# Performance work log

Measured on AMD Instinct MI355X. Metric: run time of the kernel, lower is better.

Reference implementation:

```python
import jax, jax.numpy as jnp
import numpy as np

EPS = 1e-6  # GLOBAL_EPS
D_QK = 192
ATTN_DIM = 768


def setup_inputs() -> dict:
    key = jax.random.key(0)
    ks = jax.random.split(key, 12)
    B, C, H, W = 16, 192, 56, 56
    d_qk, d_v = D_QK, 2 * D_QK
    attn_dim, inner = ATTN_DIM, d_v
    r = lambda k, s, sc=0.05: jax.random.normal(k, s, dtype=jnp.float32) * sc
    return {
        "x": jax.random.normal(ks[0], (B, C, H, W), dtype=jnp.float32),
        "proj_w": r(ks[1], (attn_dim, C)),          # 1x1 conv + BN folded
        "proj_b": r(ks[2], (attn_dim,)),
        "dwc_w": r(ks[3], (attn_dim, 1, 3, 3)),     # depthwise 3x3, BN folded
        "dwc_b": r(ks[4], (attn_dim,)),
        "g_w": r(ks[5], (inner, attn_dim)),          # ConvGate pointwise conv1d
        "g_b": r(ks[6], (inner,)),
        "an_w": 1.0 + r(ks[7], (inner,)),            # RMSNorm weight
        "sv": 1.0 + r(ks[8], (inner,)),              # Scale(inner, (1, inner, 1))
        "out_w": r(ks[9], (C, inner)),               # 1x1 conv + BN folded
        "out_b": r(ks[10], (C,)),
    }


def reference(x, proj_w, proj_b, dwc_w, dwc_b, g_w, g_b, an_w, sv, out_w, out_b):
    B, C, H, W = x.shape
    d_qk = D_QK
    # proj: ConvNorm 1x1 (conv + BN folded to affine)
    y = jnp.einsum("bchw,oc->bohw", x, proj_w) + proj_b[None, :, None, None]
    # dwc: RepConv depthwise 3x3 with residual (res=True)
    dw = jax.lax.conv_general_dilated(
        y, dwc_w, window_strides=(1, 1), padding="SAME",
        dimension_numbers=("NCHW", "OIHW", "NCHW"),
        feature_group_count=ATTN_DIM)
    y = dw + dwc_b[None, :, None, None] + y
    # flatten spatial -> tokens, split q/k/v along channels
    xs = y.reshape(B, ATTN_DIM, H * W)            # (B, attn_dim, N)
    q, k, v = xs[:, :d_qk], xs[:, d_qk:2 * d_qk], xs[:, 2 * d_qk:]
    # linear_attn: feature map = silu, scale = N**-0.5
    qf = jax.nn.silu(q)                            # (B, d_qk, N)
    kf = jax.nn.silu(k)
    N = H * W
    s = N ** -0.5
    # use_linear branch (N >> d): z = kT.mean(-2,True) @ q + eps ; attn = (v s)(kT s) q
    z = jnp.einsum("bd,bdn->bn", kf.mean(-1), qf)[:, None, :] + EPS  # (B, 1, N)
    vk = jnp.einsum("bvn,bdn->bvd", v * s, kf * s)  # (B, d_v, d_qk)
    attn = jnp.einsum("bvd,bdn->bvn", vk, qf) / z   # (B, d_v, N)
    # gate: pointwise conv1d on full projected features + sigmoid
    gate = jax.nn.sigmoid(jnp.einsum("bcn,oc->bon", xs, g_w) + g_b[None, :, None])
    attn = attn * gate
    # attn_norm (RMS over channels) + scale_v(v) residual
    rms = jnp.sqrt(jnp.mean(attn * attn, axis=1, keepdims=True) + EPS)
    attn = attn / rms * an_w[None, :, None] + v * sv[None, :, None]
    # out: ConvNorm 1x1 back to dim
    o = attn.reshape(B, -1, H, W)
    return jnp.einsum("bchw,oc->bohw", o, out_w) + out_b[None, :, None, None]
```

## Files before the change

kernel.cpp:

```cpp
#include <hip/hip_runtime.h>
#include <hip/hip_bf16.h>

typedef unsigned short u16;
typedef __attribute__((ext_vector_type(8))) short bf16x8;
typedef __attribute__((ext_vector_type(4))) float f32x4;

constexpr int B_ = 16, C_ = 192, H_ = 56, W_ = 56;
constexpr int N_ = H_ * W_;
constexpr int A_ = 768;
constexpr int Dq = 192;
constexpr int Vd = 384;
constexpr float EPSf = 1e-6f;

union U8 { bf16x8 v; u16 s[8]; unsigned u[4]; };

__device__ __forceinline__ float bits2f(u16 u) {
  return __uint_as_float(((unsigned)u) << 16);
}
__device__ __forceinline__ u16 f2bits(float f) {
  __hip_bfloat16 h = __float2bfloat16(f);
  u16 u;
  __builtin_memcpy(&u, &h, sizeof(u));
  return u;
}
__device__ __forceinline__ float silu_f(float v) { return v / (1.0f + __expf(-v)); }
__device__ __forceinline__ float sigm_f(float v) { return 1.0f / (1.0f + __expf(-v)); }

__device__ __forceinline__ f32x4 MFMA(bf16x8 a, bf16x8 b, f32x4 c) {
  return __builtin_amdgcn_mfma_f32_16x16x32_bf16(a, b, c, 0, 0, 0);
}
__device__ __forceinline__ int swz(int row) { return (row & 7) ^ ((row >> 3) & 7); }

__global__ __launch_bounds__(256) void k_prep(const float* __restrict__ pw,
                                              const float* __restrict__ gw,
                                              const float* __restrict__ ow,
                                              u16* __restrict__ pwb,
                                              u16* __restrict__ gwb,
                                              u16* __restrict__ owb) {
  const int bid = blockIdx.x;
  const size_t base = ((size_t)bid * 256 + threadIdx.x) * 8;
  const float* src;
  u16* dst;
  size_t off;
  if (bid < 72) { src = pw; dst = pwb; off = base; }
  else if (bid < 216) { src = gw; dst = gwb; off = base - 147456; }
  else { src = ow; dst = owb; off = base - 442368; }
  float4 v0 = *(const float4*)&src[off];
  float4 v1 = *(const float4*)&src[off + 4];
  U8 r;
  r.s[0] = f2bits(v0.x); r.s[1] = f2bits(v0.y); r.s[2] = f2bits(v0.z); r.s[3] = f2bits(v0.w);
  r.s[4] = f2bits(v1.x); r.s[5] = f2bits(v1.y); r.s[6] = f2bits(v1.z); r.s[7] = f2bits(v1.w);
  *(bf16x8*)&dst[off] = r.v;
}

__global__ __launch_bounds__(256) void k_proj(const float* __restrict__ x,
                                              const u16* __restrict__ pwb,
                                              const float* __restrict__ pb,
                                              u16* __restrict__ y0t) {
  const int n0 = blockIdx.x * 64;
  const int oy = blockIdx.y;
  const int b = blockIdx.z;
  __shared__ u16 Xt[64][200];
  __shared__ u16 Wa[256][32];
  const int t = threadIdx.x;
  const int lane = t & 63, wid = t >> 6;
  const int fr = lane & 15, fg = lane >> 4;

  {
    const int p = t & 31, co = t >> 5;
    const float* xb = x + (size_t)b * C_ * N_ + n0 + 2 * p;
#pragma unroll
    for (int rnd = 0; rnd < 3; ++rnd) {
      const int c0 = rnd * 64 + co * 8;
      float2 v[8];
#pragma unroll
      for (int i = 0; i < 8; ++i) v[i] = *(const float2*)&xb[(size_t)(c0 + i) * N_];
      U8 r0, r1;
#pragma unroll
      for (int i = 0; i < 8; ++i) { r0.s[i] = f2bits(v[i].x); r1.s[i] = f2bits(v[i].y); }
      *(bf16x8*)&Xt[2 * p][c0] = r0.v;
      *(bf16x8*)&Xt[2 * p + 1][c0] = r1.v;
    }
  }

  f32x4 acc[4][4];
#pragma unroll
  for (int mi = 0; mi < 4; ++mi)
#pragma unroll
    for (int ni = 0; ni < 4; ++ni) acc[mi][ni] = (f32x4){0.f, 0.f, 0.f, 0.f};

  const int orow_c = t >> 2, oct_c = t & 3;
  U8 wreg[4];
#pragma unroll
  for (int jj = 0; jj < 4; ++jj)
    wreg[jj].v = *(const bf16x8*)&pwb[(size_t)(oy * 256 + orow_c + 64 * jj) * C_ + oct_c * 8];

  for (int ks = 0; ks < 6; ++ks) {
    __syncthreads();
#pragma unroll
    for (int jj = 0; jj < 4; ++jj) {
      const int orow = orow_c + 64 * jj;
      const int sw = (orow >> 1) & 3;
      *(bf16x8*)&Wa[orow][(oct_c ^ sw) * 8] = wreg[jj].v;
    }
    __syncthreads();
    if (ks < 5) {
#pragma unroll
      for (int jj = 0; jj < 4; ++jj)
        wreg[jj].v = *(const bf16x8*)&pwb[(size_t)(oy * 256 + orow_c + 64 * jj) * C_ +
                                          (ks + 1) * 32 + oct_c * 8];
    }
    bf16x8 bfrag[4];
#pragma unroll
    for (int ni = 0; ni < 4; ++ni)
      bfrag[ni] = *(const bf16x8*)&Xt[ni * 16 + fr][ks * 32 + fg * 8];
    __builtin_amdgcn_s_setprio(1);
#pragma unroll
    for (int mi = 0; mi < 4; ++mi) {
      const int ar = wid * 64 + mi * 16 + fr;
      bf16x8 a = *(const bf16x8*)&Wa[ar][(fg ^ ((ar >> 1) & 3)) * 8];
#pragma unroll
      for (int ni = 0; ni < 4; ++ni) acc[mi][ni] = MFMA(a, bfrag[ni], acc[mi][ni]);
    }
    __builtin_amdgcn_s_setprio(0);
  }
#pragma unroll
  for (int mi = 0; mi < 4; ++mi) {
    const int o4 = oy * 256 + wid * 64 + mi * 16 + fg * 4;
    const float b0 = pb[o4], b1 = pb[o4 + 1], b2 = pb[o4 + 2], b3 = pb[o4 + 3];
#pragma unroll
    for (int ni = 0; ni < 4; ++ni) {
      const int n = n0 + ni * 16 + fr;
      ushort4 pk;
      pk.x = f2bits(acc[mi][ni][0] + b0);
      pk.y = f2bits(acc[mi][ni][1] + b1);
      pk.z = f2bits(acc[mi][ni][2] + b2);
      pk.w = f2bits(acc[mi][ni][3] + b3);
      *(ushort4*)&y0t[((size_t)b * N_ + n) * A_ + o4] = pk;
    }
  }
}

__global__ __launch_bounds__(256) void k_dwc(const u16* __restrict__ y0t,
                                             const float* __restrict__ cw,
                                             const float* __restrict__ cb,
                                             u16* __restrict__ yt) {
  const int pid = blockIdx.x;
  const int L = (pid & 7) * 336 + (pid >> 3);
  const int h = L % 56, at = (L / 56) % 3, b = L / 168;
  const int t = threadIdx.x;
  const int a = at * 256 + (t & 31) * 8;
  const int wl = t >> 5;
  float w9[9][8];
  float bias[8];
#pragma unroll
  for (int j = 0; j < 8; ++j) {
    bias[j] = cb[a + j];
#pragma unroll
    for (int k = 0; k < 9; ++k) w9[k][j] = cw[(a + j) * 9 + k];
  }
  const u16* src = y0t + (size_t)b * N_ * A_ + a;
  u16* dst = yt + (size_t)b * N_ * A_ + a;
  const bool hok0 = h > 0, hok2 = h < 55;
  for (int wc = 0; wc < 7; ++wc) {
    const int w = wc * 8 + wl;
    const bool wok0 = w > 0, wok2 = w < 55;
    U8 nb[9];
#pragma unroll
    for (int dh = -1; dh <= 1; ++dh) {
      const bool hok = (dh == -1) ? hok0 : ((dh == 1) ? hok2 : true);
#pragma unroll
      for (int dw = -1; dw <= 1; ++dw) {
        const int k = (dh + 1) * 3 + (dw + 1);
        const bool ok = hok && ((dw == -1) ? wok0 : ((dw == 1) ? wok2 : true));
        if (ok)
          nb[k].v = *(const bf16x8*)&src[(size_t)((h + dh) * 56 + (w + dw)) * A_];
        else
          nb[k].u[0] = nb[k].u[1] = nb[k].u[2] = nb[k].u[3] = 0u;
      }
    }
    U8 o;
#pragma unroll
    for (int j = 0; j < 8; ++j) {
      float s = bias[j] + bits2f(nb[4].s[j]);
#pragma unroll
      for (int k = 0; k < 9; ++k) s = fmaf(w9[k][j], bits2f(nb[k].s[j]), s);
      o.s[j] = f2bits(s);
    }
    *(bf16x8*)&dst[(size_t)(h * 56 + w) * A_] = o.v;
  }
}

__global__ __launch_bounds__(256) void k_kfmean(const u16* __restrict__ yt,
                                                float* __restrict__ kfp) {
  const int ns = blockIdx.x, dc = blockIdx.y, b = blockIdx.z;
  const int t = threadIdx.x;
  const int dq = t & 15, nw = t >> 4;
  const u16* p = yt + ((size_t)b * N_ + ns * 448 + nw) * A_ + 192 + dc * 64 + dq * 4;
  float s0 = 0, s1 = 0, s2 = 0, s3 = 0;
#pragma unroll 4
  for (int i = 0; i < 28; ++i) {
    ushort4 u = *(const ushort4*)&p[(size_t)i * 16 * A_];
    s0 += silu_f(bits2f(u.x));
    s1 += silu_f(bits2f(u.y));
    s2 += silu_f(bits2f(u.z));
    s3 += silu_f(bits2f(u.w));
  }
  __shared__ float red[16][65];
  red[nw][dq * 4 + 0] = s0;
  red[nw][dq * 4 + 1] = s1;
  red[nw][dq * 4 + 2] = s2;
  red[nw][dq * 4 + 3] = s3;
  __syncthreads();
  if (t < 64) {
    float s = 0;
#pragma unroll
    for (int i = 0; i < 16; ++i) s += red[i][t];
    kfp[((size_t)ns * B_ + b) * Dq + dc * 64 + t] = s * (1.0f / (float)N_);
  }
}

__global__ __launch_bounds__(256) void k_z(const u16* __restrict__ yt,
                                           const float* __restrict__ kfp,
                                           float* __restrict__ zinv) {
  const int b = blockIdx.y;
  const int n = blockIdx.x * 256 + threadIdx.x;
  __shared__ float kf[192];
  if (threadIdx.x < 192) {
    float s = 0;
#pragma unroll
    for (int ns = 0; ns < 7; ++ns) s += kfp[((size_t)ns * B_ + b) * Dq + threadIdx.x];
    kf[threadIdx.x] = s;
  }
  __syncthreads();
  if (n < N_) {
    const u16* p = yt + ((size_t)b * N_ + n) * A_;
    float z = 0;
#pragma unroll
    for (int j = 0; j < 24; ++j) {
      U8 u;
      u.v = *(const bf16x8*)&p[j * 8];
#pragma unroll
      for (int i = 0; i < 8; ++i) z = fmaf(kf[j * 8 + i], silu_f(bits2f(u.s[i])), z);
    }
    zinv[(size_t)b * N_ + n] = 1.0f / (z + EPSf);
  }
}

__global__ __launch_bounds__(256) void k_vk(const u16* __restrict__ yt,
                                            float* __restrict__ vkpart) {
  const int pid = blockIdx.x;
  const int L = (pid & 7) * 42 + (pid >> 3);
  const int ns = L % 7;
  const int vblk = (L / 7) % 3;
  const int b = L / 21;
  const int t = threadIdx.x;
  const int lane = t & 63, wid = t >> 6;
  const int fr = lane & 15, fg = lane >> 4;
  const int vbase = (wid >> 1) * 64, dbase = (wid & 1) * 96;

  __shared__ u16 T[320 * 64];
  unsigned* T32 = (unsigned*)T;

  const int oct0 = t & 7;
  const int pair = (t >> 3) & 31;
  const int nb0 = ns * 448;

  U8 pre[5][2];
  auto load_pre = [&](int n0) {
    const int n = nb0 + n0 + pair * 2;
#pragma unroll
    for (int j = 0; j < 5; ++j) {
      const int oct = oct0 + 8 * j;
      const u16* srcp;
      if (j < 3)
        srcp = yt + ((size_t)b * N_ + n) * A_ + 192 + oct * 8;
      else
        srcp = yt + ((size_t)b * N_ + n) * A_ + 384 + vblk * 128 + (oct - 24) * 8;
      pre[j][0].v = *(const bf16x8*)srcp;
      pre[j][1].v = *(const bf16x8*)(srcp + A_);
      if (j < 3) {
#pragma unroll
        for (int i = 0; i < 8; ++i) {
          pre[j][0].s[i] = f2bits(silu_f(bits2f(pre[j][0].s[i])));
          pre[j][1].s[i] = f2bits(silu_f(bits2f(pre[j][1].s[i])));
        }
      }
    }
  };

  f32x4 acc[4][6];
#pragma unroll
  for (int mi = 0; mi < 4; ++mi)
#pragma unroll
    for (int ni = 0; ni < 6; ++ni) acc[mi][ni] = (f32x4){0.f, 0.f, 0.f, 0.f};

  load_pre(0);
  for (int s = 0; s < 7; ++s) {
    __syncthreads();
#pragma unroll
    for (int j = 0; j < 5; ++j) {
      const int rowb = (oct0 + 8 * j) * 8;
#pragma unroll
      for (int i = 0; i < 8; ++i) {
        const int row = rowb + i;
        const int sw = swz(row);
        const unsigned val =
            ((unsigned)pre[j][0].s[i] & 0xffffu) | (((unsigned)pre[j][1].s[i]) << 16);
        T32[row * 32 + (pair ^ (sw << 2))] = val;
      }
    }
    __syncthreads();
    if (s < 6) load_pre((s + 1) * 64);
    __builtin_amdgcn_s_setprio(1);
#pragma unroll
    for (int kf2 = 0; kf2 < 2; ++kf2) {
      bf16x8 bfrag[6];
#pragma unroll
      for (int ni = 0; ni < 6; ++ni) {
        const int row = dbase + ni * 16 + fr;
        bfrag[ni] = *(const bf16x8*)&T[row * 64 + ((kf2 * 32 + fg * 8) ^ (swz(row) << 3))];
      }
#pragma unroll
      for (int mi = 0; mi < 4; ++mi) {
        const int row = 192 + vbase + mi * 16 + fr;
        bf16x8 a = *(const bf16x8*)&T[row * 64 + ((kf2 * 32 + fg * 8) ^ (swz(row) << 3))];
#pragma unroll
        for (int ni = 0; ni < 6; ++ni) acc[mi][ni] = MFMA(a, bfrag[ni], acc[mi][ni]);
      }
    }
    __builtin_amdgcn_s_setprio(0);
  }
  float* base = vkpart + (((size_t)ns * 16 + b) * 3 + vblk) * (128 * 192);
#pragma unroll
  for (int mi = 0; mi < 4; ++mi)
#pragma unroll
    for (int ni = 0; ni < 6; ++ni) {
      const int v = vbase + mi * 16 + fg * 4;
      const int d = dbase + ni * 16 + fr;
      float* o = base + (size_t)v * 192 + d;
      o[0] = acc[mi][ni][0];
      o[192] = acc[mi][ni][1];
      o[384] = acc[mi][ni][2];
      o[576] = acc[mi][ni][3];
    }
}

__global__ __launch_bounds__(256) void k_vkred(const float* __restrict__ vkpart,
                                               u16* __restrict__ vkb) {
  const size_t e = ((size_t)blockIdx.x * 256 + threadIdx.x) * 8;
  constexpr size_t NSSTRIDE = (size_t)16 * 3 * 128 * 192;
  float4 s0 = {0, 0, 0, 0}, s1 = {0, 0, 0, 0};
#pragma unroll
  for (int ns = 0; ns < 7; ++ns) {
    float4 a0 = *(const float4*)&vkpart[ns * NSSTRIDE + e];
    float4 a1 = *(const float4*)&vkpart[ns * NSSTRIDE + e + 4];
    s0.x += a0.x; s0.y += a0.y; s0.z += a0.z; s0.w += a0.w;
    s1.x += a1.x; s1.y += a1.y; s1.z += a1.z; s1.w += a1.w;
  }
  const float sc = 1.0f / (float)N_;
  U8 r;
  r.s[0] = f2bits(s0.x * sc); r.s[1] = f2bits(s0.y * sc);
  r.s[2] = f2bits(s0.z * sc); r.s[3] = f2bits(s0.w * sc);
  r.s[4] = f2bits(s1.x * sc); r.s[5] = f2bits(s1.y * sc);
  r.s[6] = f2bits(s1.z * sc); r.s[7] = f2bits(s1.w * sc);
  *(bf16x8*)&vkb[e] = r.v;
}

__global__ __launch_bounds__(256) void k_gateattn(const u16* __restrict__ yt,
                                                  const float* __restrict__ zinv,
                                                  const u16* __restrict__ vkb,
                                                  const u16* __restrict__ gwb,
                                                  const float* __restrict__ gb,
                                                  u16* __restrict__ attnt) {
  const int pid = blockIdx.x;
  const int L = (pid & 7) * 196 + (pid >> 3);
  const int vh = L & 1;
  const int n0 = ((L >> 1) % 49) * 64;
  const int b = L / 98;
  const int t = threadIdx.x;
  const int lane = t & 63, wid = t >> 6, wm = wid >> 1, wn = wid & 1;
  const int fr = lane & 15, fg = lane >> 4;
  __shared__ u16 T[2][256 * 64];
  __shared__ float zl[64];
  if (t < 64) zl[t] = zinv[(size_t)b * N_ + n0 + t];
  const u16* yb = yt + ((size_t)b * N_ + n0) * A_;
  const u16* wb0 = vkb + ((size_t)b * Vd + vh * 192) * 192;
  const u16* wb1 = gwb + (size_t)(vh * 192) * A_;

  const int oct = t & 7, rowb = t >> 3;
  U8 pre[8];
  auto loadPre = [&](int nit) {
    if (nit < 3) {
      const int ks = nit * 64;
#pragma unroll
      for (int j = 0; j < 6; ++j)
        pre[j].v = *(const bf16x8*)&wb0[(size_t)(rowb + 32 * j) * 192 + ks + oct * 8];
#pragma unroll
      for (int j = 6; j < 8; ++j)
        pre[j].v = *(const bf16x8*)&yb[(size_t)(rowb + 32 * (j - 6)) * A_ + ks + oct * 8];
    } else {
      const int ks = (nit - 3) * 64;
#pragma unroll
      for (int j = 0; j < 6; ++j)
        pre[j].v = *(const bf16x8*)&wb1[(size_t)(rowb + 32 * j) * A_ + ks + oct * 8];
#pragma unroll
      for (int j = 6; j < 8; ++j)
        pre[j].v = *(const bf16x8*)&yb[(size_t)(rowb + 32 * (j - 6)) * A_ + ks + oct * 8];
    }
  };
  auto writeStage = [&](int nit, int buf) {
    const bool sl = (nit < 3);
    u16* Tb = &T[buf][0];
#pragma unroll
    for (int j = 0; j < 8; ++j) {
      const int r = rowb + 32 * j;
      U8 w = pre[j];
      if (sl && j >= 6) {
#pragma unroll
        for (int i = 0; i < 8; ++i) w.s[i] = f2bits(silu_f(bits2f(w.s[i])));
      }
      *(bf16x8*)&Tb[r * 64 + ((oct * 8) ^ (swz(r) << 3))] = w.v;
    }
  };

  f32x4 acc[6][2];
#pragma unroll
  for (int mi = 0; mi < 6; ++mi)
#pragma unroll
    for (int ni = 0; ni < 2; ++ni) acc[mi][ni] = (f32x4){0.f, 0.f, 0.f, 0.f};
  uint2 pp[6][2];

  loadPre(0);
  writeStage(0, 0);
  loadPre(1);
  __syncthreads();

  for (int it = 0; it < 15; ++it) {
    const int cur = it & 1;
    if (it < 14) writeStage(it + 1, cur ^ 1);
    if (it < 13) loadPre(it + 2);
    const u16* Tb = &T[cur][0];
    __builtin_amdgcn_s_setprio(1);
#pragma unroll
    for (int kf2 = 0; kf2 < 2; ++kf2) {
      bf16x8 bfr[2];
#pragma unroll
      for (int ni = 0; ni < 2; ++ni) {
        const int row = 192 + wn * 32 + ni * 16 + fr;
        bfr[ni] = *(const bf16x8*)&Tb[row * 64 + ((kf2 * 32 + fg * 8) ^ (swz(row) << 3))];
      }
#pragma unroll
      for (int mi = 0; mi < 6; ++mi) {
        const int row = wm * 96 + mi * 16 + fr;
        bf16x8 a = *(const bf16x8*)&Tb[row * 64 + ((kf2 * 32 + fg * 8) ^ (swz(row) << 3))];
        acc[mi][0] = MFMA(a, bfr[0], acc[mi][0]);
        acc[mi][1] = MFMA(a, bfr[1], acc[mi][1]);
      }
    }
    __builtin_amdgcn_s_setprio(0);
    if (it == 2) {
#pragma unroll
      for (int mi = 0; mi < 6; ++mi)
#pragma unroll
        for (int ni = 0; ni < 2; ++ni) {
          const float z = zl[wn * 32 + ni * 16 + fr];
          unsigned a0 = ((unsigned)f2bits(acc[mi][ni][0] * z) & 0xffffu) |
                        (((unsigned)f2bits(acc[mi][ni][1] * z) & 0xffffu) << 16);
          unsigned a1 = ((unsigned)f2bits(acc[mi][ni][2] * z) & 0xffffu) |
                        (((unsigned)f2bits(acc[mi][ni][3] * z) & 0xffffu) << 16);
          pp[mi][ni] = make_uint2(a0, a1);
          acc[mi][ni] = (f32x4){0.f, 0.f, 0.f, 0.f};
        }
    }
    __syncthreads();
  }

#pragma unroll
  for (int mi = 0; mi < 6; ++mi) {
    const int vb = vh * 192 + wm * 96 + mi * 16 + fg * 4;
    const float g0 = gb[vb], g1 = gb[vb + 1], g2 = gb[vb + 2], g3 = gb[vb + 3];
#pragma unroll
    for (int ni = 0; ni < 2; ++ni) {
      const int n = n0 + wn * 32 + ni * 16 + fr;
      const uint2 p = pp[mi][ni];
      const float pv0 = bits2f((u16)(p.x & 0xffffu)), pv1 = bits2f((u16)(p.x >> 16));
      const float pv2 = bits2f((u16)(p.y & 0xffffu)), pv3 = bits2f((u16)(p.y >> 16));
      ushort4 o;
      o.x = f2bits(pv0 * sigm_f(acc[mi][ni][0] + g0));
      o.y = f2bits(pv1 * sigm_f(acc[mi][ni][1] + g1));
      o.z = f2bits(pv2 * sigm_f(acc[mi][ni][2] + g2));
      o.w = f2bits(pv3 * sigm_f(acc[mi][ni][3] + g3));
      *(ushort4*)&attnt[((size_t)b * N_ + n) * Vd + vb] = o;
    }
  }
}

__global__ __launch_bounds__(256) void k_out(const u16* __restrict__ attnt,
                                             const u16* __restrict__ yt,
                                             const u16* __restrict__ owb,
                                             const float* __restrict__ ob,
                                             const float* __restrict__ anw,
                                             const float* __restrict__ svw,
                                             float* __restrict__ out) {
  const int n0 = blockIdx.x * 64;
  const int b = blockIdx.y;
  __shared__ u16 T[256 * 64];
  __shared__ float anws[384], svws[384];
  __shared__ float red[64][4];
  __shared__ float rinv[64];
  const int t = threadIdx.x;
  const int lane = t & 63, wid = t >> 6, wm = wid >> 1, wn = wid & 1;
  const int fr = lane & 15, fg = lane >> 4;
  for (int i = t; i < 384; i += 256) {
    anws[i] = anw[i];
    svws[i] = svw[i];
  }
  {
    const int n = t >> 2, q = t & 3;
    const u16* ab = attnt + ((size_t)b * N_ + n0 + n) * Vd;
    float ss = 0.f;
#pragma unroll
    for (int i = 0; i < 4; ++i) {
      U8 u, u2, u3;
      u.v = *(const bf16x8*)&ab[(q + 4 * i) * 8 + 0];
      u2.v = *(const bf16x8*)&ab[(q + 4 * i) * 8 + 128];
      u3.v = *(const bf16x8*)&ab[(q + 4 * i) * 8 + 256];
#pragma unroll
      for (int k = 0; k < 8; ++k) {
        float f0 = bits2f(u.s[k]), f1 = bits2f(u2.s[k]), f2 = bits2f(u3.s[k]);
        ss = fmaf(f0, f0, ss);
        ss = fmaf(f1, f1, ss);
        ss = fmaf(f2, f2, ss);
      }
    }
    red[n][q] = ss;
  }
  __syncthreads();
  if (t < 64)
    rinv[t] = rsqrtf((red[t][0] + red[t][1] + red[t][2] + red[t][3]) * (1.0f / (float)Vd) + EPSf);

  const int oct = t & 7, rowb = t >> 3;
  U8 preW[6], preA[2], preV[2];
  auto loadPre = [&](int it) {
    const int ks = it * 64;
#pragma unroll
    for (int j = 0; j < 6; ++j)
      preW[j].v = *(const bf16x8*)&owb[(size_t)(rowb + 32 * j) * Vd + ks + oct * 8];
#pragma unroll
    for (int j = 0; j < 2; ++j) {
      const int n = rowb + 32 * j;
      preA[j].v = *(const bf16x8*)&attnt[((size_t)b * N_ + n0 + n) * Vd + ks + oct * 8];
      preV[j].v = *(const bf16x8*)&yt[((size_t)b * N_ + n0 + n) * A_ + 384 + ks + oct * 8];
    }
  };

  f32x4 acc[6][2];
#pragma unroll
  for (int mi = 0; mi < 6; ++mi)
#pragma unroll
    for (int ni = 0; ni < 2; ++ni) acc[mi][ni] = (f32x4){0.f, 0.f, 0.f, 0.f};

  loadPre(0);
  __syncthreads();
  for (int it = 0; it < 6; ++it) {
#pragma unroll
    for (int j = 0; j < 6; ++j) {
      const int r = rowb + 32 * j;
      *(bf16x8*)&T[r * 64 + ((oct * 8) ^ (swz(r) << 3))] = preW[j].v;
    }
#pragma unroll
    for (int j = 0; j < 2; ++j) {
      const int n = rowb + 32 * j;
      const int r = 192 + n;
      const float ri = rinv[n];
      const int col0 = it * 64 + oct * 8;
      U8 o;
#pragma unroll
      for (int k = 0; k < 8; ++k)
        o.s[k] = f2bits(bits2f(preA[j].s[k]) * ri * anws[col0 + k] +
                        bits2f(preV[j].s[k]) * svws[col0 + k]);
      *(bf16x8*)&T[r * 64 + ((oct * 8) ^ (swz(r) << 3))] = o.v;
    }
    __syncthreads();
    if (it < 5) loadPre(it + 1);
    __builtin_amdgcn_s_setprio(1);
#pragma unroll
    for (int kf2 = 0; kf2 < 2; ++kf2) {
      bf16x8 bfr[2];
#pragma unroll
      for (int ni = 0; ni < 2; ++ni) {
        const int row = 192 + wn * 32 + ni * 16 + fr;
        bfr[ni] = *(const bf16x8*)&T[row * 64 + ((kf2 * 32 + fg * 8) ^ (swz(row) << 3))];
      }
#pragma unroll
      for (int mi = 0; mi < 6; ++mi) {
        const int row = wm * 96 + mi * 16 + fr;
        bf16x8 a = *(const bf16x8*)&T[row * 64 + ((kf2 * 32 + fg * 8) ^ (swz(row) << 3))];
        acc[mi][0] = MFMA(a, bfr[0], acc[mi][0]);
        acc[mi][1] = MFMA(a, bfr[1], acc[mi][1]);
      }
    }
    __builtin_amdgcn_s_setprio(0);
    if (it < 5) __syncthreads();
  }
#pragma unroll
  for (int mi = 0; mi < 6; ++mi) {
    const int c = wm * 96 + mi * 16 + fg * 4;
    const float b0 = ob[c], b1 = ob[c + 1], b2 = ob[c + 2], b3 = ob[c + 3];
#pragma unroll
    for (int ni = 0; ni < 2; ++ni) {
      const int n = n0 + wn * 32 + ni * 16 + fr;
      float* o = out + ((size_t)b * C_ + c) * N_ + n;
      o[0 * N_] = acc[mi][ni][0] + b0;
      o[1 * N_] = acc[mi][ni][1] + b1;
      o[2 * N_] = acc[mi][ni][2] + b2;
      o[3 * N_] = acc[mi][ni][3] + b3;
    }
  }
}

extern "C" void kernel_launch(void* const* d_in, const int* in_sizes, int n_in,
                              void* d_out, int out_size, void* d_ws, size_t ws_size,
                              hipStream_t stream) {
  (void)in_sizes; (void)n_in; (void)out_size; (void)ws_size;
  const float* x = (const float*)d_in[0];
  const float* pw = (const float*)d_in[1];
  const float* pb = (const float*)d_in[2];
  const float* cw = (const float*)d_in[3];
  const float* cb = (const float*)d_in[4];
  const float* gw = (const float*)d_in[5];
  const float* gb = (const float*)d_in[6];
  const float* anw = (const float*)d_in[7];
  const float* svw = (const float*)d_in[8];
  const float* ow = (const float*)d_in[9];
  const float* ob = (const float*)d_in[10];
  float* out = (float*)d_out;

  char* ws = (char*)d_ws;
  const size_t szY = (size_t)B_ * N_ * A_ * 2;
  u16* y0t = (u16*)(ws);
  u16* attnt = (u16*)(ws);
  float* vkpart = (float*)(ws + 38535168);
  u16* vkb = (u16*)(ws + 71565312);
  u16* yt = (u16*)(ws + szY);
  char* ws2 = ws + 2 * szY;
  float* kfp = (float*)(ws2);
  float* zinv = (float*)(ws2 + 86016);
  u16* pwb = (u16*)(ws2 + 86016 + 200704);
  u16* gwb = (u16*)(ws2 + 86016 + 200704 + 294912);
  u16* owb = (u16*)(ws2 + 86016 + 200704 + 294912 + 589824);

  k_prep<<<dim3(252), 256, 0, stream>>>(pw, gw, ow, pwb, gwb, owb);
  k_proj<<<dim3(49, 3, 16), 256, 0, stream>>>(x, pwb, pb, y0t);
  k_dwc<<<dim3(2688), 256, 0, stream>>>(y0t, cw, cb, yt);
  k_kfmean<<<dim3(7, 3, 16), 256, 0, stream>>>(yt, kfp);
  k_z<<<dim3(13, 16), 256, 0, stream>>>(yt, kfp, zinv);
  k_vk<<<dim3(336), 256, 0, stream>>>(yt, vkpart);
  k_vkred<<<dim3(576), 256, 0, stream>>>(vkpart, vkb);
  k_gateattn<<<dim3(1568), 256, 0, stream>>>(yt, zinv, vkb, gwb, gb, attnt);
  k_out<<<dim3(49, 16), 256, 0, stream>>>(attnt, yt, owb, ob, anw, svw, out);
}
```

Before: 264.3 us.

## Widen gate-attention token tile to 128 and fuse RMS sum-of-squares via atomics

The per-batch token stride is padded to 3200 so the gate/attention kernel can use 128-token tiles (800 blocks instead of 1568), doubling MFMA columns per wave and halving how often weight tiles are reloaded. The gate kernel now accumulates each token's sum of squares and adds it atomically into a buffer, which k_z zeroes beforehand. This removes the separate re-read of the attention output in k_out for the RMS norm. In exchange it needs more registers and LDS per block (launch bounds 2), computes on padded tokens (whose zinv is set to zero), and uses float atomics, so the summation order is no longer fixed.

```diff
diff --git a/kernel.cpp b/kernel.cpp
--- a/kernel.cpp
+++ b/kernel.cpp
@@ -7,6 +7,7 @@
 
 constexpr int B_ = 16, C_ = 192, H_ = 56, W_ = 56;
 constexpr int N_ = H_ * W_;
+constexpr int NP = 3200;
 constexpr int A_ = 768;
 constexpr int Dq = 192;
 constexpr int Vd = 384;
@@ -136,7 +137,7 @@
       pk.y = f2bits(acc[mi][ni][1] + b1);
       pk.z = f2bits(acc[mi][ni][2] + b2);
       pk.w = f2bits(acc[mi][ni][3] + b3);
-      *(ushort4*)&y0t[((size_t)b * N_ + n) * A_ + o4] = pk;
+      *(ushort4*)&y0t[((size_t)b * NP + n) * A_ + o4] = pk;
     }
   }
 }
@@ -159,8 +160,8 @@
 #pragma unroll
     for (int k = 0; k < 9; ++k) w9[k][j] = cw[(a + j) * 9 + k];
   }
-  const u16* src = y0t + (size_t)b * N_ * A_ + a;
-  u16* dst = yt + (size_t)b * N_ * A_ + a;
+  const u16* src = y0t + (size_t)b * NP * A_ + a;
+  u16* dst = yt + (size_t)b * NP * A_ + a;
   const bool hok0 = h > 0, hok2 = h < 55;
   for (int wc = 0; wc < 7; ++wc) {
     const int w = wc * 8 + wl;
@@ -196,7 +197,7 @@
   const int ns = blockIdx.x, dc = blockIdx.y, b = blockIdx.z;
   const int t = threadIdx.x;
   const int dq = t & 15, nw = t >> 4;
-  const u16* p = yt + ((size_t)b * N_ + ns * 448 + nw) * A_ + 192 + dc * 64 + dq * 4;
+  const u16* p = yt + ((size_t)b * NP + ns * 448 + nw) * A_ + 192 + dc * 64 + dq * 4;
   float s0 = 0, s1 = 0, s2 = 0, s3 = 0;
 #pragma unroll 4
   for (int i = 0; i < 28; ++i) {
@@ -222,7 +223,8 @@
 
 __global__ __launch_bounds__(256) void k_z(const u16* __restrict__ yt,
                                            const float* __restrict__ kfp,
-                                           float* __restrict__ zinv) {
+                                           float* __restrict__ zinv,
+                                           float* __restrict__ ssq) {
   const int b = blockIdx.y;
   const int n = blockIdx.x * 256 + threadIdx.x;
   __shared__ float kf[192];
@@ -233,17 +235,22 @@
     kf[threadIdx.x] = s;
   }
   __syncthreads();
-  if (n < N_) {
-    const u16* p = yt + ((size_t)b * N_ + n) * A_;
-    float z = 0;
-#pragma unroll
-    for (int j = 0; j < 24; ++j) {
-      U8 u;
-      u.v = *(const bf16x8*)&p[j * 8];
-#pragma unroll
-      for (int i = 0; i < 8; ++i) z = fmaf(kf[j * 8 + i], silu_f(bits2f(u.s[i])), z);
-    }
-    zinv[(size_t)b * N_ + n] = 1.0f / (z + EPSf);
+  if (n < NP) {
+    if (n < N_) {
+      const u16* p = yt + ((size_t)b * NP + n) * A_;
+      float z = 0;
+#pragma unroll
+      for (int j = 0; j < 24; ++j) {
+        U8 u;
+        u.v = *(const bf16x8*)&p[j * 8];
+#pragma unroll
+        for (int i = 0; i < 8; ++i) z = fmaf(kf[j * 8 + i], silu_f(bits2f(u.s[i])), z);
+      }
+      zinv[(size_t)b * NP + n] = 1.0f / (z + EPSf);
+    } else {
+      zinv[(size_t)b * NP + n] = 0.f;
+    }
+    ssq[(size_t)b * NP + n] = 0.f;
   }
 }
 
@@ -274,9 +281,9 @@
       const int oct = oct0 + 8 * j;
       const u16* srcp;
       if (j < 3)
-        srcp = yt + ((size_t)b * N_ + n) * A_ + 192 + oct * 8;
+        srcp = yt + ((size_t)b * NP + n) * A_ + 192 + oct * 8;
       else
-        srcp = yt + ((size_t)b * N_ + n) * A_ + 384 + vblk * 128 + (oct - 24) * 8;
+        srcp = yt + ((size_t)b * NP + n) * A_ + 384 + vblk * 128 + (oct - 24) * 8;
       pre[j][0].v = *(const bf16x8*)srcp;
       pre[j][1].v = *(const bf16x8*)(srcp + A_);
       if (j < 3) {
@@ -367,29 +374,28 @@
   *(bf16x8*)&vkb[e] = r.v;
 }
 
-__global__ __launch_bounds__(256) void k_gateattn(const u16* __restrict__ yt,
-                                                  const float* __restrict__ zinv,
-                                                  const u16* __restrict__ vkb,
-                                                  const u16* __restrict__ gwb,
-                                                  const float* __restrict__ gb,
-                                                  u16* __restrict__ attnt) {
+__global__ __launch_bounds__(256, 2) void k_gateattn(const u16* __restrict__ yt,
+                                                     const float* __restrict__ zinv,
+                                                     const u16* __restrict__ vkb,
+                                                     const u16* __restrict__ gwb,
+                                                     const float* __restrict__ gb,
+                                                     u16* __restrict__ attnt,
+                                                     float* __restrict__ ssq) {
   const int pid = blockIdx.x;
-  const int L = (pid & 7) * 196 + (pid >> 3);
+  const int L = (pid & 7) * 100 + (pid >> 3);
   const int vh = L & 1;
-  const int n0 = ((L >> 1) % 49) * 64;
-  const int b = L / 98;
+  const int n0 = ((L >> 1) % 25) * 128;
+  const int b = L / 50;
   const int t = threadIdx.x;
   const int lane = t & 63, wid = t >> 6, wm = wid >> 1, wn = wid & 1;
   const int fr = lane & 15, fg = lane >> 4;
-  __shared__ u16 T[2][256 * 64];
-  __shared__ float zl[64];
-  if (t < 64) zl[t] = zinv[(size_t)b * N_ + n0 + t];
-  const u16* yb = yt + ((size_t)b * N_ + n0) * A_;
+  __shared__ u16 T[2][320 * 64];
+  const u16* yb = yt + ((size_t)b * NP + n0) * A_;
   const u16* wb0 = vkb + ((size_t)b * Vd + vh * 192) * 192;
   const u16* wb1 = gwb + (size_t)(vh * 192) * A_;
 
   const int oct = t & 7, rowb = t >> 3;
-  U8 pre[8];
+  U8 pre[10];
   auto loadPre = [&](int nit) {
     if (nit < 3) {
       const int ks = nit * 64;
@@ -397,7 +403,7 @@
       for (int j = 0; j < 6; ++j)
         pre[j].v = *(const bf16x8*)&wb0[(size_t)(rowb + 32 * j) * 192 + ks + oct * 8];
 #pragma unroll
-      for (int j = 6; j < 8; ++j)
+      for (int j = 6; j < 10; ++j)
         pre[j].v = *(const bf16x8*)&yb[(size_t)(rowb + 32 * (j - 6)) * A_ + ks + oct * 8];
     } else {
       const int ks = (nit - 3) * 64;
@@ -405,7 +411,7 @@
       for (int j = 0; j < 6; ++j)
         pre[j].v = *(const bf16x8*)&wb1[(size_t)(rowb + 32 * j) * A_ + ks + oct * 8];
 #pragma unroll
-      for (int j = 6; j < 8; ++j)
+      for (int j = 6; j < 10; ++j)
         pre[j].v = *(const bf16x8*)&yb[(size_t)(rowb + 32 * (j - 6)) * A_ + ks + oct * 8];
     }
   };
@@ -413,7 +419,7 @@
     const bool sl = (nit < 3);
     u16* Tb = &T[buf][0];
 #pragma unroll
-    for (int j = 0; j < 8; ++j) {
+    for (int j = 0; j < 10; ++j) {
       const int r = rowb + 32 * j;
       U8 w = pre[j];
       if (sl && j >= 6) {
@@ -424,12 +430,12 @@
     }
   };
 
-  f32x4 acc[6][2];
+  f32x4 acc[6][4];
 #pragma unroll
   for (int mi = 0; mi < 6; ++mi)
 #pragma unroll
-    for (int ni = 0; ni < 2; ++ni) acc[mi][ni] = (f32x4){0.f, 0.f, 0.f, 0.f};
-  uint2 pp[6][2];
+    for (int ni = 0; ni < 4; ++ni) acc[mi][ni] = (f32x4){0.f, 0.f, 0.f, 0.f};
+  uint2 pp[6][4];
 
   loadPre(0);
   writeStage(0, 0);
@@ -444,27 +450,31 @@
     __builtin_amdgcn_s_setprio(1);
 #pragma unroll
     for (int kf2 = 0; kf2 < 2; ++kf2) {
-      bf16x8 bfr[2];
-#pragma unroll
-      for (int ni = 0; ni < 2; ++ni) {
-        const int row = 192 + wn * 32 + ni * 16 + fr;
+      bf16x8 bfr[4];
+#pragma unroll
+      for (int ni = 0; ni < 4; ++ni) {
+        const int row = 192 + wn * 64 + ni * 16 + fr;
         bfr[ni] = *(const bf16x8*)&Tb[row * 64 + ((kf2 * 32 + fg * 8) ^ (swz(row) << 3))];
       }
 #pragma unroll
       for (int mi = 0; mi < 6; ++mi) {
         const int row = wm * 96 + mi * 16 + fr;
         bf16x8 a = *(const bf16x8*)&Tb[row * 64 + ((kf2 * 32 + fg * 8) ^ (swz(row) << 3))];
-        acc[mi][0] = MFMA(a, bfr[0], acc[mi][0]);
-        acc[mi][1] = MFMA(a, bfr[1], acc[mi][1]);
+#pragma unroll
+        for (int ni = 0; ni < 4; ++ni) acc[mi][ni] = MFMA(a, bfr[ni], acc[mi][ni]);
       }
     }
     __builtin_amdgcn_s_setprio(0);
     if (it == 2) {
+      float zv[4];
+#pragma unroll
+      for (int ni = 0; ni < 4; ++ni)
+        zv[ni] = zinv[(size_t)b * NP + n0 + wn * 64 + ni * 16 + fr];
 #pragma unroll
       for (int mi = 0; mi < 6; ++mi)
 #pragma unroll
-        for (int ni = 0; ni < 2; ++ni) {
-          const float z = zl[wn * 32 + ni * 16 + fr];
+        for (int ni = 0; ni < 4; ++ni) {
+          const float z = zv[ni];
           unsigned a0 = ((unsigned)f2bits(acc[mi][ni][0] * z) & 0xffffu) |
                         (((unsigned)f2bits(acc[mi][ni][1] * z) & 0xffffu) << 16);
           unsigned a1 = ((unsigned)f2bits(acc[mi][ni][2] * z) & 0xffffu) |
@@ -476,22 +486,38 @@
     __syncthreads();
   }
 
+  float ssqa[4] = {0.f, 0.f, 0.f, 0.f};
 #pragma unroll
   for (int mi = 0; mi < 6; ++mi) {
     const int vb = vh * 192 + wm * 96 + mi * 16 + fg * 4;
     const float g0 = gb[vb], g1 = gb[vb + 1], g2 = gb[vb + 2], g3 = gb[vb + 3];
 #pragma unroll
-    for (int ni = 0; ni < 2; ++ni) {
-      const int n = n0 + wn * 32 + ni * 16 + fr;
+    for (int ni = 0; ni < 4; ++ni) {
+      const int n = n0 + wn * 64 + ni * 16 + fr;
       const uint2 p = pp[mi][ni];
       const float pv0 = bits2f((u16)(p.x & 0xffffu)), pv1 = bits2f((u16)(p.x >> 16));
       const float pv2 = bits2f((u16)(p.y & 0xffffu)), pv3 = bits2f((u16)(p.y >> 16));
+      const float q0 = pv0 * sigm_f(acc[mi][ni][0] + g0);
+      const float q1 = pv1 * sigm_f(acc[mi][ni][1] + g1);
+      const float q2 = pv2 * sigm_f(acc[mi][ni][2] + g2);
+      const float q3 = pv3 * sigm_f(acc[mi][ni][3] + g3);
       ushort4 o;
-      o.x = f2bits(pv0 * sigm_f(acc[mi][ni][0] + g0));
-      o.y = f2bits(pv1 * sigm_f(acc[mi][ni][1] + g1));
-      o.z = f2bits(pv2 * sigm_f(acc[mi][ni][2] + g2));
-      o.w = f2bits(pv3 * sigm_f(acc[mi][ni][3] + g3));
-      *(ushort4*)&attnt[((size_t)b * N_ + n) * Vd + vb] = o;
+      o.x = f2bits(q0);
+      o.y = f2bits(q1);
+      o.z = f2bits(q2);
+      o.w = f2bits(q3);
+      *(ushort4*)&attnt[((size_t)b * NP + n) * Vd + vb] = o;
+      ssqa[ni] += q0 * q0 + q1 * q1 + q2 * q2 + q3 * q3;
+    }
+  }
+#pragma unroll
+  for (int ni = 0; ni < 4; ++ni) {
+    float ss = ssqa[ni];
+    ss += __shfl_xor(ss, 16);
+    ss += __shfl_xor(ss, 32);
+    if (fg == 0) {
+      const int n = n0 + wn * 64 + ni * 16 + fr;
+      atomicAdd(&ssq[(size_t)b * NP + n], ss);
     }
   }
 }
@@ -502,12 +528,12 @@
                                              const float* __restrict__ ob,
                                              const float* __restrict__ anw,
                                              const float* __restrict__ svw,
+                                             const float* __restrict__ ssq,
                                              float* __restrict__ out) {
   const int n0 = blockIdx.x * 64;
   const int b = blockIdx.y;
   __shared__ u16 T[256 * 64];
   __shared__ float anws[384], svws[384];
-  __shared__ float red[64][4];
   __shared__ float rinv[64];
   const int t = threadIdx.x;
   const int lane = t & 63, wid = t >> 6, wm = wid >> 1, wn = wid & 1;
@@ -516,29 +542,8 @@
     anws[i] = anw[i];
     svws[i] = svw[i];
   }
-  {
-    const int n = t >> 2, q = t & 3;
-    const u16* ab = attnt + ((size_t)b * N_ + n0 + n) * Vd;
-    float ss = 0.f;
-#pragma unroll
-    for (int i = 0; i < 4; ++i) {
-      U8 u, u2, u3;
-      u.v = *(const bf16x8*)&ab[(q + 4 * i) * 8 + 0];
-      u2.v = *(const bf16x8*)&ab[(q + 4 * i) * 8 + 128];
-      u3.v = *(const bf16x8*)&ab[(q + 4 * i) * 8 + 256];
-#pragma unroll
-      for (int k = 0; k < 8; ++k) {
-        float f0 = bits2f(u.s[k]), f1 = bits2f(u2.s[k]), f2 = bits2f(u3.s[k]);
-        ss = fmaf(f0, f0, ss);
-        ss = fmaf(f1, f1, ss);
-        ss = fmaf(f2, f2, ss);
-      }
-    }
-    red[n][q] = ss;
-  }
-  __syncthreads();
   if (t < 64)
-    rinv[t] = rsqrtf((red[t][0] + red[t][1] + red[t][2] + red[t][3]) * (1.0f / (float)Vd) + EPSf);
+    rinv[t] = rsqrtf(ssq[(size_t)b * NP + n0 + t] * (1.0f / (float)Vd) + EPSf);
 
   const int oct = t & 7, rowb = t >> 3;
   U8 preW[6], preA[2], preV[2];
@@ -550,8 +555,8 @@
 #pragma unroll
     for (int j = 0; j < 2; ++j) {
       const int n = rowb + 32 * j;
-      preA[j].v = *(const bf16x8*)&attnt[((size_t)b * N_ + n0 + n) * Vd + ks + oct * 8];
-      preV[j].v = *(const bf16x8*)&yt[((size_t)b * N_ + n0 + n) * A_ + 384 + ks + oct * 8];
+      preA[j].v = *(const bf16x8*)&attnt[((size_t)b * NP + n0 + n) * Vd + ks + oct * 8];
+      preV[j].v = *(const bf16x8*)&yt[((size_t)b * NP + n0 + n) * A_ + 384 + ks + oct * 8];
     }
   };
 
@@ -638,26 +643,27 @@
   float* out = (float*)d_out;
 
   char* ws = (char*)d_ws;
-  const size_t szY = (size_t)B_ * N_ * A_ * 2;
+  const size_t szY = (size_t)B_ * NP * A_ * 2;
   u16* y0t = (u16*)(ws);
   u16* attnt = (u16*)(ws);
-  float* vkpart = (float*)(ws + 38535168);
-  u16* vkb = (u16*)(ws + 71565312);
+  float* vkpart = (float*)(ws + 39321600);
+  u16* vkb = (u16*)(ws + 72351744);
   u16* yt = (u16*)(ws + szY);
   char* ws2 = ws + 2 * szY;
   float* kfp = (float*)(ws2);
   float* zinv = (float*)(ws2 + 86016);
-  u16* pwb = (u16*)(ws2 + 86016 + 200704);
-  u16* gwb = (u16*)(ws2 + 86016 + 200704 + 294912);
-  u16* owb = (u16*)(ws2 + 86016 + 200704 + 294912 + 589824);
+  float* ssq = (float*)(ws2 + 86016 + 204800);
+  u16* pwb = (u16*)(ws2 + 86016 + 2 * 204800);
+  u16* gwb = (u16*)(ws2 + 86016 + 2 * 204800 + 294912);
+  u16* owb = (u16*)(ws2 + 86016 + 2 * 204800 + 294912 + 589824);
 
   k_prep<<<dim3(252), 256, 0, stream>>>(pw, gw, ow, pwb, gwb, owb);
   k_proj<<<dim3(49, 3, 16), 256, 0, stream>>>(x, pwb, pb, y0t);
   k_dwc<<<dim3(2688), 256, 0, stream>>>(y0t, cw, cb, yt);
   k_kfmean<<<dim3(7, 3, 16), 256, 0, stream>>>(yt, kfp);
-  k_z<<<dim3(13, 16), 256, 0, stream>>>(yt, kfp, zinv);
+  k_z<<<dim3(13, 16), 256, 0, stream>>>(yt, kfp, zinv, ssq);
   k_vk<<<dim3(336), 256, 0, stream>>>(yt, vkpart);
   k_vkred<<<dim3(576), 256, 0, stream>>>(vkpart, vkb);
-  k_gateattn<<<dim3(1568), 256, 0, stream>>>(yt, zinv, vkb, gwb, gb, attnt);
-  k_out<<<dim3(49, 16), 256, 0, stream>>>(attnt, yt, owb, ob, anw, svw, out);
-}
+  k_gateattn<<<dim3(800), 256, 0, stream>>>(yt, zinv, vkb, gwb, gb, attnt, ssq);
+  k_out<<<dim3(49, 16), 256, 0, stream>>>(attnt, yt, owb, ob, anw, svw, ssq, out);
+}
```

Result: slower. 296.4 us (+12.1%).

## Fuse silu(k) mean reduction into depthwise conv and reuse sliding columns

Applied to the files above, without the earlier changes.

The separate k_kfmean kernel is removed. The depthwise conv now accumulates silu of the k channels in registers, reduces them per block in shared memory and atomically adds the sums into a zeroed kfp buffer; k_prep gains an extra block that does the zeroing. The conv loop also changes so each thread walks 7 consecutive columns and keeps a 3-column window, loading one new column per output instead of nine neighbours. This saves a full re-read of the k slice and one launch, at the cost of float atomics whose summation order is not deterministic, and it uses the fp32 conv value rather than the bf16-rounded one.

```diff
diff --git a/kernel.cpp b/kernel.cpp
--- a/kernel.cpp
+++ b/kernel.cpp
@@ -36,8 +36,13 @@
                                               const float* __restrict__ ow,
                                               u16* __restrict__ pwb,
                                               u16* __restrict__ gwb,
-                                              u16* __restrict__ owb) {
+                                              u16* __restrict__ owb,
+                                              float* __restrict__ kfp) {
   const int bid = blockIdx.x;
+  if (bid == 252) {
+    for (int i = threadIdx.x; i < B_ * Dq; i += 256) kfp[i] = 0.f;
+    return;
+  }
   const size_t base = ((size_t)bid * 256 + threadIdx.x) * 8;
   const float* src;
   u16* dst;
@@ -144,13 +149,14 @@
 __global__ __launch_bounds__(256) void k_dwc(const u16* __restrict__ y0t,
                                              const float* __restrict__ cw,
                                              const float* __restrict__ cb,
-                                             u16* __restrict__ yt) {
+                                             u16* __restrict__ yt,
+                                             float* __restrict__ kfp) {
   const int pid = blockIdx.x;
   const int L = (pid & 7) * 336 + (pid >> 3);
   const int h = L % 56, at = (L / 56) % 3, b = L / 168;
   const int t = threadIdx.x;
   const int a = at * 256 + (t & 31) * 8;
-  const int wl = t >> 5;
+  const int ws0 = (t >> 5) * 7;
   float w9[9][8];
   float bias[8];
 #pragma unroll
@@ -162,61 +168,61 @@
   const u16* src = y0t + (size_t)b * N_ * A_ + a;
   u16* dst = yt + (size_t)b * N_ * A_ + a;
   const bool hok0 = h > 0, hok2 = h < 55;
-  for (int wc = 0; wc < 7; ++wc) {
-    const int w = wc * 8 + wl;
-    const bool wok0 = w > 0, wok2 = w < 55;
-    U8 nb[9];
-#pragma unroll
-    for (int dh = -1; dh <= 1; ++dh) {
-      const bool hok = (dh == -1) ? hok0 : ((dh == 1) ? hok2 : true);
-#pragma unroll
-      for (int dw = -1; dw <= 1; ++dw) {
-        const int k = (dh + 1) * 3 + (dw + 1);
-        const bool ok = hok && ((dw == -1) ? wok0 : ((dw == 1) ? wok2 : true));
-        if (ok)
-          nb[k].v = *(const bf16x8*)&src[(size_t)((h + dh) * 56 + (w + dw)) * A_];
-        else
-          nb[k].u[0] = nb[k].u[1] = nb[k].u[2] = nb[k].u[3] = 0u;
-      }
-    }
+
+  U8 cm[3], cc[3], cp[3];
+  auto zero8 = [](U8& x) { x.u[0] = x.u[1] = x.u[2] = x.u[3] = 0u; };
+  auto loadcol = [&](U8 col[3], int w) {
+    if ((unsigned)w < 56u) {
+      if (hok0) col[0].v = *(const bf16x8*)&src[(size_t)((h - 1) * 56 + w) * A_];
+      else zero8(col[0]);
+      col[1].v = *(const bf16x8*)&src[(size_t)(h * 56 + w) * A_];
+      if (hok2) col[2].v = *(const bf16x8*)&src[(size_t)((h + 1) * 56 + w) * A_];
+      else zero8(col[2]);
+    } else {
+      zero8(col[0]); zero8(col[1]); zero8(col[2]);
+    }
+  };
+  loadcol(cm, ws0 - 1);
+  loadcol(cc, ws0);
+
+  float kacc[8] = {0.f, 0.f, 0.f, 0.f, 0.f, 0.f, 0.f, 0.f};
+#pragma unroll
+  for (int i = 0; i < 7; ++i) {
+    const int w = ws0 + i;
+    loadcol(cp, w + 1);
     U8 o;
 #pragma unroll
     for (int j = 0; j < 8; ++j) {
-      float s = bias[j] + bits2f(nb[4].s[j]);
-#pragma unroll
-      for (int k = 0; k < 9; ++k) s = fmaf(w9[k][j], bits2f(nb[k].s[j]), s);
+      float s = bias[j] + bits2f(cc[1].s[j]);
+      s = fmaf(w9[0][j], bits2f(cm[0].s[j]), s);
+      s = fmaf(w9[1][j], bits2f(cc[0].s[j]), s);
+      s = fmaf(w9[2][j], bits2f(cp[0].s[j]), s);
+      s = fmaf(w9[3][j], bits2f(cm[1].s[j]), s);
+      s = fmaf(w9[4][j], bits2f(cc[1].s[j]), s);
+      s = fmaf(w9[5][j], bits2f(cp[1].s[j]), s);
+      s = fmaf(w9[6][j], bits2f(cm[2].s[j]), s);
+      s = fmaf(w9[7][j], bits2f(cc[2].s[j]), s);
+      s = fmaf(w9[8][j], bits2f(cp[2].s[j]), s);
       o.s[j] = f2bits(s);
+      const int ch = a + j;
+      if (ch >= 192 && ch < 384) kacc[j] += silu_f(s);
     }
     *(bf16x8*)&dst[(size_t)(h * 56 + w) * A_] = o.v;
-  }
-}
-
-__global__ __launch_bounds__(256) void k_kfmean(const u16* __restrict__ yt,
-                                                float* __restrict__ kfp) {
-  const int ns = blockIdx.x, dc = blockIdx.y, b = blockIdx.z;
-  const int t = threadIdx.x;
-  const int dq = t & 15, nw = t >> 4;
-  const u16* p = yt + ((size_t)b * N_ + ns * 448 + nw) * A_ + 192 + dc * 64 + dq * 4;
-  float s0 = 0, s1 = 0, s2 = 0, s3 = 0;
-#pragma unroll 4
-  for (int i = 0; i < 28; ++i) {
-    ushort4 u = *(const ushort4*)&p[(size_t)i * 16 * A_];
-    s0 += silu_f(bits2f(u.x));
-    s1 += silu_f(bits2f(u.y));
-    s2 += silu_f(bits2f(u.z));
-    s3 += silu_f(bits2f(u.w));
-  }
-  __shared__ float red[16][65];
-  red[nw][dq * 4 + 0] = s0;
-  red[nw][dq * 4 + 1] = s1;
-  red[nw][dq * 4 + 2] = s2;
-  red[nw][dq * 4 + 3] = s3;
-  __syncthreads();
-  if (t < 64) {
-    float s = 0;
-#pragma unroll
-    for (int i = 0; i < 16; ++i) s += red[i][t];
-    kfp[((size_t)ns * B_ + b) * Dq + dc * 64 + t] = s * (1.0f / (float)N_);
+#pragma unroll
+    for (int r = 0; r < 3; ++r) { cm[r] = cc[r]; cc[r] = cp[r]; }
+  }
+
+  __shared__ float red[8][256];
+  if (at < 2) {
+    const int cbase = (t & 31) * 8, wl = t >> 5;
+#pragma unroll
+    for (int j = 0; j < 8; ++j) red[wl][cbase + j] = kacc[j];
+    __syncthreads();
+    float s = 0.f;
+#pragma unroll
+    for (int i = 0; i < 8; ++i) s += red[i][t];
+    const int ac = at * 256 + t;
+    if (ac >= 192 && ac < 384) atomicAdd(&kfp[b * Dq + (ac - 192)], s);
   }
 }
 
@@ -226,12 +232,8 @@
   const int b = blockIdx.y;
   const int n = blockIdx.x * 256 + threadIdx.x;
   __shared__ float kf[192];
-  if (threadIdx.x < 192) {
-    float s = 0;
-#pragma unroll
-    for (int ns = 0; ns < 7; ++ns) s += kfp[((size_t)ns * B_ + b) * Dq + threadIdx.x];
-    kf[threadIdx.x] = s;
-  }
+  if (threadIdx.x < 192)
+    kf[threadIdx.x] = kfp[b * Dq + threadIdx.x] * (1.0f / (float)N_);
   __syncthreads();
   if (n < N_) {
     const u16* p = yt + ((size_t)b * N_ + n) * A_;
@@ -651,10 +653,9 @@
   u16* gwb = (u16*)(ws2 + 86016 + 200704 + 294912);
   u16* owb = (u16*)(ws2 + 86016 + 200704 + 294912 + 589824);
 
-  k_prep<<<dim3(252), 256, 0, stream>>>(pw, gw, ow, pwb, gwb, owb);
+  k_prep<<<dim3(253), 256, 0, stream>>>(pw, gw, ow, pwb, gwb, owb, kfp);
   k_proj<<<dim3(49, 3, 16), 256, 0, stream>>>(x, pwb, pb, y0t);
-  k_dwc<<<dim3(2688), 256, 0, stream>>>(y0t, cw, cb, yt);
-  k_kfmean<<<dim3(7, 3, 16), 256, 0, stream>>>(yt, kfp);
+  k_dwc<<<dim3(2688), 256, 0, stream>>>(y0t, cw, cb, yt, kfp);
   k_z<<<dim3(13, 16), 256, 0, stream>>>(yt, kfp, zinv);
   k_vk<<<dim3(336), 256, 0, stream>>>(yt, vkpart);
   k_vkred<<<dim3(576), 256, 0, stream>>>(vkpart, vkb);
```

Result: no change. 264.0 us (-0.1%).
